# Kernel optimization log

Hardware: AMD Instinct MI355X
Metric: run time of the kernel (lower is better)

## Reference

```python
import jax, jax.numpy as jnp
import numpy as np

EPS = 1e-6
NUM_HEADS = 16


def _layer_norm(x):
    # LayerNorm32: fp32 layernorm, eps=1e-6, no affine params
    m = jnp.mean(x, axis=-1, keepdims=True)
    v = jnp.var(x, axis=-1, keepdims=True)
    return (x - m) * jax.lax.rsqrt(v + EPS)


def setup_inputs() -> dict:
    key = jax.random.key(0)
    ks = jax.random.split(key, 6)
    B, L, C = 4, 2048, 1024
    H = 4 * C
    s = 0.02
    return {
        "x": jax.random.normal(ks[0], (B, L, C), dtype=jnp.float32),
        "qkv_w": jax.random.normal(ks[1], (C, 3 * C), dtype=jnp.float32) * s,
        "qkv_b": jnp.zeros((3 * C,), dtype=jnp.float32),
        "proj_w": jax.random.normal(ks[2], (C, C), dtype=jnp.float32) * s,
        "proj_b": jnp.zeros((C,), dtype=jnp.float32),
        "fc1_w": jax.random.normal(ks[3], (C, H), dtype=jnp.float32) * s,
        "fc1_b": jnp.zeros((H,), dtype=jnp.float32),
        "fc2_w": jax.random.normal(ks[4], (H, C), dtype=jnp.float32) * s,
        "fc2_b": jnp.zeros((C,), dtype=jnp.float32),
    }


def _block(x, qkv_w, qkv_b, proj_w, proj_b, fc1_w, fc1_b, fc2_w, fc2_b):
    B, L, C = x.shape
    Hn = NUM_HEADS
    D = C // Hn

    # --- attention branch (pre-norm) ---
    h = _layer_norm(x)
    qkv = h @ qkv_w + qkv_b                      # [B, L, 3C]
    qkv = qkv.reshape(B, L, 3, Hn, D)
    q, k, v = qkv[:, :, 0], qkv[:, :, 1], qkv[:, :, 2]  # [B, L, Hn, D]
    scale = 1.0 / jnp.sqrt(jnp.asarray(D, dtype=x.dtype))
    logits = jnp.einsum("bqhd,bkhd->bhqk", q, k) * scale
    attn = jax.nn.softmax(logits, axis=-1)
    o = jnp.einsum("bhqk,bkhd->bqhd", attn, v).reshape(B, L, C)
    o = o @ proj_w + proj_b
    x = x + o

    # --- MLP branch (pre-norm) ---
    h = _layer_norm(x)
    h = jax.nn.gelu(h @ fc1_w + fc1_b, approximate=True)  # tanh GELU
    h = h @ fc2_w + fc2_b
    return x + h


def reference(x, qkv_w, qkv_b, proj_w, proj_b, fc1_w, fc1_b, fc2_w, fc2_b):
    return _block(x, qkv_w, qkv_b, proj_w, proj_b, fc1_w, fc1_b, fc2_w, fc2_b)
```

## Files before the change

### kernel.cpp

```cpp
#include <hip/hip_runtime.h>
#include <hip/hip_bf16.h>

typedef float f32x4 __attribute__((ext_vector_type(4)));
typedef __bf16 bf16x8 __attribute__((ext_vector_type(8)));
typedef unsigned short us8 __attribute__((ext_vector_type(8)));

#define MBYTE (1ull << 20)

#define QSCALE_LOG2E 0.18033688011112042f

__device__ __forceinline__ unsigned short f2bf(float f) {
    unsigned int u = __float_as_uint(f);
    u += 0x7fffu + ((u >> 16) & 1u);
    return (unsigned short)(u >> 16);
}

__device__ __forceinline__ float fast_exp2(float x) {
    return __builtin_amdgcn_exp2f(x);
}

__device__ __forceinline__ f32x4 mfma16(bf16x8 a, bf16x8 b, f32x4 c) {
    return __builtin_amdgcn_mfma_f32_16x16x32_bf16(a, b, c, 0, 0, 0);
}

__device__ __forceinline__ void gload16(const void* g, void* l) {
    __builtin_amdgcn_global_load_lds(
        (const __attribute__((address_space(1))) unsigned int*)g,
        (__attribute__((address_space(3))) unsigned int*)l, 16, 0, 0);
}

__global__ __launch_bounds__(256) void ln_kernel(const float* __restrict__ x,
                                                 unsigned short* __restrict__ out) {
    int row = blockIdx.x;
    int t = threadIdx.x;
    const float* xr = x + (size_t)row * 1024;
    float4 v = *(const float4*)(xr + t * 4);
    float s = v.x + v.y + v.z + v.w;
    float ss = v.x * v.x + v.y * v.y + v.z * v.z + v.w * v.w;
    #pragma unroll
    for (int off = 1; off < 64; off <<= 1) {
        s += __shfl_xor(s, off);
        ss += __shfl_xor(ss, off);
    }
    __shared__ float ps[4], pss[4];
    int wid = t >> 6, lane = t & 63;
    if (lane == 0) { ps[wid] = s; pss[wid] = ss; }
    __syncthreads();
    s = ps[0] + ps[1] + ps[2] + ps[3];
    ss = pss[0] + pss[1] + pss[2] + pss[3];
    float mean = s * (1.0f / 1024.0f);
    float var = ss * (1.0f / 1024.0f) - mean * mean;
    float rs = rsqrtf(var + 1e-6f);
    ushort4 ov;
    ov.x = f2bf((v.x - mean) * rs);
    ov.y = f2bf((v.y - mean) * rs);
    ov.z = f2bf((v.z - mean) * rs);
    ov.w = f2bf((v.w - mean) * rs);
    *(ushort4*)(out + (size_t)row * 1024 + t * 4) = ov;
}

__global__ __launch_bounds__(256) void convT_kernel(const float* __restrict__ W,
                                                    unsigned short* __restrict__ Wt,
                                                    int K, int N) {
    __shared__ float tile[32][33];
    int t = threadIdx.x;
    int tx = t & 31, ty = t >> 5;
    int bx = blockIdx.x, by = blockIdx.y;
    #pragma unroll
    for (int r = 0; r < 4; r++) {
        int row = by * 32 + ty + r * 8;
        int col = bx * 32 + tx;
        tile[ty + r * 8][tx] = W[(size_t)row * N + col];
    }
    __syncthreads();
    #pragma unroll
    for (int r = 0; r < 4; r++) {
        int orow = bx * 32 + ty + r * 8;
        int ocol = by * 32 + tx;
        Wt[(size_t)orow * K + ocol] = f2bf(tile[tx][ty + r * 8]);
    }
}

__global__ __launch_bounds__(256) void vT_kernel(const unsigned short* __restrict__ qkv,
                                                 unsigned short* __restrict__ vT) {
    __shared__ unsigned short tile[32][34];
    int t = threadIdx.x;
    int tx = t & 31, ty = t >> 5;
    int lt = blockIdx.x, dt = blockIdx.y, bh = blockIdx.z;
    int b = bh >> 4, h = bh & 15;
    const unsigned short* src = qkv + (size_t)(b * 2048 + lt * 32) * 3072 + 2048 + h * 64 + dt * 32;
    #pragma unroll
    for (int r = 0; r < 4; r++)
        tile[ty + r * 8][tx] = src[(size_t)(ty + r * 8) * 3072 + tx];
    __syncthreads();
    int perm = (lt & 1) * 32 + ((tx >> 2) & 3) * 8 + ((tx >> 4) & 1) * 4 + (tx & 3);
    unsigned short* dst = vT + ((size_t)bh * 64 + dt * 32) * 2048 + (size_t)(lt >> 1) * 64;
    #pragma unroll
    for (int r = 0; r < 4; r++)
        dst[(size_t)(ty + r * 8) * 2048 + perm] = tile[tx][ty + r * 8];
}

template <int EPI>
__global__ __launch_bounds__(256) void gemm_bt(const unsigned short* __restrict__ A,
                                               const unsigned short* __restrict__ Bt,
                                               const float* __restrict__ bias,
                                               const float* __restrict__ res,
                                               float* __restrict__ outF,
                                               unsigned short* __restrict__ outB,
                                               int M, int N, int K) {
    __shared__ __align__(16) unsigned short As[128 * 32];
    __shared__ __align__(16) unsigned short Bs[128 * 32];
    int t = threadIdx.x;
    int lane = t & 63, wid = t >> 6;

    int gx = gridDim.x;
    int nwg = gx * gridDim.y;
    int orig = blockIdx.y * gx + blockIdx.x;
    int cpx = nwg >> 3;
    int swz = (orig & 7) * cpx + (orig >> 3);
    int bm = swz / gx, bn = swz % gx;

    int wm = wid >> 1, wn = wid & 1;
    f32x4 acc[4][4] = {};

    int sub = lane >> 2;
    int chunk = lane & 3;
    const unsigned short* gA0 = A + (size_t)(bm * 128 + wid * 32 + sub) * K + chunk * 8;
    const unsigned short* gA1 = gA0 + (size_t)16 * K;
    const unsigned short* gB0 = Bt + (size_t)(bn * 128 + wid * 32 + sub) * K + chunk * 8;
    const unsigned short* gB1 = gB0 + (size_t)16 * K;
    unsigned short* lA0 = &As[(wid * 32) * 32];
    unsigned short* lA1 = &As[(wid * 32 + 16) * 32];
    unsigned short* lB0 = &Bs[(wid * 32) * 32];
    unsigned short* lB1 = &Bs[(wid * 32 + 16) * 32];

    for (int k0 = 0; k0 < K; k0 += 32) {
        __syncthreads();
        gload16(gA0 + k0, lA0);
        gload16(gA1 + k0, lA1);
        gload16(gB0 + k0, lB0);
        gload16(gB1 + k0, lB1);
        __syncthreads();
        bf16x8 af[4], bfr[4];
        #pragma unroll
        for (int m = 0; m < 4; m++)
            af[m] = *(const bf16x8*)&As[(wm * 64 + m * 16 + (lane & 15)) * 32 + (lane >> 4) * 8];
        #pragma unroll
        for (int n = 0; n < 4; n++)
            bfr[n] = *(const bf16x8*)&Bs[(wn * 64 + n * 16 + (lane & 15)) * 32 + (lane >> 4) * 8];
        #pragma unroll
        for (int m = 0; m < 4; m++)
            #pragma unroll
            for (int n = 0; n < 4; n++)
                acc[m][n] = mfma16(af[m], bfr[n], acc[m][n]);
    }

    #pragma unroll
    for (int m = 0; m < 4; m++) {
        #pragma unroll
        for (int n = 0; n < 4; n++) {
            int col = bn * 128 + wn * 64 + n * 16 + (lane & 15);
            float bv = bias[col];
            #pragma unroll
            for (int r = 0; r < 4; r++) {
                int row = bm * 128 + wm * 64 + m * 16 + (lane >> 4) * 4 + r;
                float val = acc[m][n][r] + bv;
                if (EPI == 0) {
                    if (col < 1024) val *= QSCALE_LOG2E;
                    outB[(size_t)row * N + col] = f2bf(val);
                } else if (EPI == 1) {
                    float g = 0.5f * val *
                              (1.0f + tanhf(0.7978845608028654f *
                                            (val + 0.044715f * val * val * val)));
                    outB[(size_t)row * N + col] = f2bf(g);
                } else {
                    outF[(size_t)row * N + col] = val + res[(size_t)row * N + col];
                }
            }
        }
    }
}

__global__ __launch_bounds__(256) void attn_kernel(const unsigned short* __restrict__ qkv,
                                                   const unsigned short* __restrict__ vT,
                                                   unsigned short* __restrict__ o) {
    int bid = blockIdx.x;
    int qb = bid & 31;
    int bh = bid >> 5;
    int b = bh >> 4, h = bh & 15;
    int t = threadIdx.x, lane = t & 63, wid = t >> 6;

    const unsigned short* base = qkv + (size_t)b * 2048 * 3072 + h * 64;
    const unsigned short* vbase = vT + (size_t)bh * 64 * 2048;

    __shared__ __align__(16) unsigned short Ks[64][72];
    __shared__ __align__(16) unsigned short Vs[64][72];

    int ql = lane & 15;
    int hi = lane >> 4;

    bf16x8 qf[2];
    {
        int qrow = qb * 64 + wid * 16 + ql;
        const unsigned short* qp = base + (size_t)qrow * 3072 + hi * 8;
        qf[0] = *(const bf16x8*)(qp);
        qf[1] = *(const bf16x8*)(qp + 32);
    }

    float m_r = -1e30f, lpart = 0.0f;
    f32x4 accO[4] = {};

    int srow = t >> 2;
    int scol = (t & 3) * 16;
    const unsigned short* kp = base + 1024 + (size_t)srow * 3072 + scol;
    const unsigned short* vp = vbase + (size_t)srow * 2048 + scol;

    us8 kr0 = *(const us8*)kp;
    us8 kr1 = *(const us8*)(kp + 8);
    us8 vr0 = *(const us8*)vp;
    us8 vr1 = *(const us8*)(vp + 8);

    for (int kt = 0; kt < 32; kt++) {
        __syncthreads();
        *(us8*)&Ks[srow][scol] = kr0;
        *(us8*)&Ks[srow][scol + 8] = kr1;
        *(us8*)&Vs[srow][scol] = vr0;
        *(us8*)&Vs[srow][scol + 8] = vr1;
        if (kt + 1 < 32) {
            const unsigned short* kpn = kp + (size_t)(kt + 1) * 64 * 3072;
            const unsigned short* vpn = vp + (kt + 1) * 64;
            kr0 = *(const us8*)kpn;
            kr1 = *(const us8*)(kpn + 8);
            vr0 = *(const us8*)vpn;
            vr1 = *(const us8*)(vpn + 8);
        }
        __syncthreads();

        f32x4 s0 = {}, s1 = {}, s2 = {}, s3 = {};
        #pragma unroll
        for (int c = 0; c < 2; c++) {
            bf16x8 a0 = *(const bf16x8*)&Ks[ 0 + ql][c * 32 + hi * 8];
            bf16x8 a1 = *(const bf16x8*)&Ks[16 + ql][c * 32 + hi * 8];
            bf16x8 a2 = *(const bf16x8*)&Ks[32 + ql][c * 32 + hi * 8];
            bf16x8 a3 = *(const bf16x8*)&Ks[48 + ql][c * 32 + hi * 8];
            s0 = mfma16(a0, qf[c], s0);
            s1 = mfma16(a1, qf[c], s1);
            s2 = mfma16(a2, qf[c], s2);
            s3 = mfma16(a3, qf[c], s3);
        }

        float mx = fmaxf(fmaxf(fmaxf(s0[0], s0[1]), fmaxf(s0[2], s0[3])),
                         fmaxf(fmaxf(s1[0], s1[1]), fmaxf(s1[2], s1[3])));
        mx = fmaxf(mx, fmaxf(fmaxf(s2[0], s2[1]), fmaxf(s2[2], s2[3])));
        mx = fmaxf(mx, fmaxf(fmaxf(s3[0], s3[1]), fmaxf(s3[2], s3[3])));
        if (!__all(mx <= m_r + 8.0f)) {
            float mm = fmaxf(mx, __shfl_xor(mx, 16));
            mm = fmaxf(mm, __shfl_xor(mm, 32));
            float mnew = fmaxf(m_r, mm);
            float corr = fast_exp2(m_r - mnew);
            m_r = mnew;
            lpart *= corr;
            #pragma unroll
            for (int r = 0; r < 4; r++) {
                float cq = __shfl(corr, hi * 4 + r);
                accO[0][r] *= cq; accO[1][r] *= cq;
                accO[2][r] *= cq; accO[3][r] *= cq;
            }
        }

        us8 pu0, pu1;
        #pragma unroll
        for (int j = 0; j < 4; j++) {
            float pa = fast_exp2(s0[j] - m_r);
            float pb = fast_exp2(s1[j] - m_r);
            float pc = fast_exp2(s2[j] - m_r);
            float pd = fast_exp2(s3[j] - m_r);
            lpart += (pa + pb) + (pc + pd);
            pu0[j] = f2bf(pa); pu0[4 + j] = f2bf(pb);
            pu1[j] = f2bf(pc); pu1[4 + j] = f2bf(pd);
        }
        bf16x8 paf0 = __builtin_bit_cast(bf16x8, pu0);
        bf16x8 paf1 = __builtin_bit_cast(bf16x8, pu1);

        #pragma unroll
        for (int nn = 0; nn < 4; nn++) {
            bf16x8 bv0 = *(const bf16x8*)&Vs[nn * 16 + ql][hi * 8];
            bf16x8 bv1 = *(const bf16x8*)&Vs[nn * 16 + ql][32 + hi * 8];
            accO[nn] = mfma16(paf0, bv0, accO[nn]);
            accO[nn] = mfma16(paf1, bv1, accO[nn]);
        }
    }

    lpart += __shfl_xor(lpart, 16);
    lpart += __shfl_xor(lpart, 32);
    float rinv = 1.0f / lpart;
    #pragma unroll
    for (int r = 0; r < 4; r++) {
        float rq = __shfl(rinv, hi * 4 + r);
        int row = qb * 64 + wid * 16 + hi * 4 + r;
        #pragma unroll
        for (int nn = 0; nn < 4; nn++) {
            int col = h * 64 + nn * 16 + ql;
            o[(size_t)(b * 2048 + row) * 1024 + col] = f2bf(accO[nn][r] * rq);
        }
    }
}

extern "C" void kernel_launch(void* const* d_in, const int* in_sizes, int n_in,
                              void* d_out, int out_size, void* d_ws, size_t ws_size,
                              hipStream_t stream) {
    const float* x      = (const float*)d_in[0];
    const float* qkv_w  = (const float*)d_in[1];
    const float* qkv_b  = (const float*)d_in[2];
    const float* proj_w = (const float*)d_in[3];
    const float* proj_b = (const float*)d_in[4];
    const float* fc1_w  = (const float*)d_in[5];
    const float* fc1_b  = (const float*)d_in[6];
    const float* fc2_w  = (const float*)d_in[7];
    const float* fc2_b  = (const float*)d_in[8];
    float* out = (float*)d_out;

    char* ws = (char*)d_ws;
    unsigned short* h_buf   = (unsigned short*)(ws + 0 * MBYTE);
    unsigned short* qkv_buf = (unsigned short*)(ws + 16 * MBYTE);
    unsigned short* o_buf   = (unsigned short*)(ws + 64 * MBYTE);
    float*          x2_buf  = (float*)(ws + 80 * MBYTE);
    unsigned short* vT_buf  = (unsigned short*)(ws + 80 * MBYTE);
    unsigned short* wqT     = (unsigned short*)(ws + 112 * MBYTE);
    unsigned short* wpT     = (unsigned short*)(ws + 118 * MBYTE);
    unsigned short* w1T     = (unsigned short*)(ws + 120 * MBYTE);
    unsigned short* w2T     = (unsigned short*)(ws + 128 * MBYTE);
    unsigned short* g_buf   = (unsigned short*)(ws + 16 * MBYTE);

    const int M = 8192;

    convT_kernel<<<dim3(3072 / 32, 1024 / 32), 256, 0, stream>>>(qkv_w, wqT, 1024, 3072);
    convT_kernel<<<dim3(1024 / 32, 1024 / 32), 256, 0, stream>>>(proj_w, wpT, 1024, 1024);
    convT_kernel<<<dim3(4096 / 32, 1024 / 32), 256, 0, stream>>>(fc1_w, w1T, 1024, 4096);
    convT_kernel<<<dim3(1024 / 32, 4096 / 32), 256, 0, stream>>>(fc2_w, w2T, 4096, 1024);

    ln_kernel<<<M, 256, 0, stream>>>(x, h_buf);

    gemm_bt<0><<<dim3(3072 / 128, M / 128), 256, 0, stream>>>(
        h_buf, wqT, qkv_b, nullptr, nullptr, qkv_buf, M, 3072, 1024);

    vT_kernel<<<dim3(64, 2, 64), 256, 0, stream>>>(qkv_buf, vT_buf);

    attn_kernel<<<dim3(32 * 64), 256, 0, stream>>>(qkv_buf, vT_buf, o_buf);

    gemm_bt<2><<<dim3(1024 / 128, M / 128), 256, 0, stream>>>(
        o_buf, wpT, proj_b, x, x2_buf, nullptr, M, 1024, 1024);

    ln_kernel<<<M, 256, 0, stream>>>(x2_buf, h_buf);

    gemm_bt<1><<<dim3(4096 / 128, M / 128), 256, 0, stream>>>(
        h_buf, w1T, fc1_b, nullptr, nullptr, g_buf, M, 4096, 1024);

    gemm_bt<2><<<dim3(1024 / 128, M / 128), 256, 0, stream>>>(
        g_buf, w2T, fc2_b, x2_buf, out, nullptr, M, 1024, 4096);
}
```

Baseline: 481.7 us.

## Load K/V tiles directly into LDS with global_load_lds and split layout

```diff
diff --git a/kernel.cpp b/kernel.cpp
--- a/kernel.cpp
+++ b/kernel.cpp
@@ -10,9 +10,8 @@
 #define QSCALE_LOG2E 0.18033688011112042f
 
 __device__ __forceinline__ unsigned short f2bf(float f) {
-    unsigned int u = __float_as_uint(f);
-    u += 0x7fffu + ((u >> 16) & 1u);
-    return (unsigned short)(u >> 16);
+    __bf16 h = (__bf16)f;
+    return __builtin_bit_cast(unsigned short, h);
 }
 
 __device__ __forceinline__ float fast_exp2(float x) {
@@ -193,8 +192,8 @@
     const unsigned short* base = qkv + (size_t)b * 2048 * 3072 + h * 64;
     const unsigned short* vbase = vT + (size_t)bh * 64 * 2048;
 
-    __shared__ __align__(16) unsigned short Ks[64][72];
-    __shared__ __align__(16) unsigned short Vs[64][72];
+    __shared__ __align__(16) unsigned short Ks[2][64][32];
+    __shared__ __align__(16) unsigned short Vs[2][64][32];
 
     int ql = lane & 15;
     int hi = lane >> 4;
@@ -210,39 +209,32 @@
     float m_r = -1e30f, lpart = 0.0f;
     f32x4 accO[4] = {};
 
-    int srow = t >> 2;
-    int scol = (t & 3) * 16;
-    const unsigned short* kp = base + 1024 + (size_t)srow * 3072 + scol;
-    const unsigned short* vp = vbase + (size_t)srow * 2048 + scol;
-
-    us8 kr0 = *(const us8*)kp;
-    us8 kr1 = *(const us8*)(kp + 8);
-    us8 vr0 = *(const us8*)vp;
-    us8 vr1 = *(const us8*)(vp + 8);
+    int srow = wid * 16 + (lane >> 2);
+    int schunk = (lane & 3) * 8;
+    const unsigned short* gk = base + 1024 + (size_t)srow * 3072 + schunk;
+    const unsigned short* gv = vbase + (size_t)srow * 2048 + schunk;
+    unsigned short* lK0 = &Ks[0][wid * 16][0];
+    unsigned short* lK1 = &Ks[1][wid * 16][0];
+    unsigned short* lV0 = &Vs[0][wid * 16][0];
+    unsigned short* lV1 = &Vs[1][wid * 16][0];
 
     for (int kt = 0; kt < 32; kt++) {
         __syncthreads();
-        *(us8*)&Ks[srow][scol] = kr0;
-        *(us8*)&Ks[srow][scol + 8] = kr1;
-        *(us8*)&Vs[srow][scol] = vr0;
-        *(us8*)&Vs[srow][scol + 8] = vr1;
-        if (kt + 1 < 32) {
-            const unsigned short* kpn = kp + (size_t)(kt + 1) * 64 * 3072;
-            const unsigned short* vpn = vp + (kt + 1) * 64;
-            kr0 = *(const us8*)kpn;
-            kr1 = *(const us8*)(kpn + 8);
-            vr0 = *(const us8*)vpn;
-            vr1 = *(const us8*)(vpn + 8);
-        }
+        gload16(gk, lK0);
+        gload16(gk + 32, lK1);
+        gload16(gv, lV0);
+        gload16(gv + 32, lV1);
+        gk += (size_t)64 * 3072;
+        gv += 64;
         __syncthreads();
 
         f32x4 s0 = {}, s1 = {}, s2 = {}, s3 = {};
         #pragma unroll
         for (int c = 0; c < 2; c++) {
-            bf16x8 a0 = *(const bf16x8*)&Ks[ 0 + ql][c * 32 + hi * 8];
-            bf16x8 a1 = *(const bf16x8*)&Ks[16 + ql][c * 32 + hi * 8];
-            bf16x8 a2 = *(const bf16x8*)&Ks[32 + ql][c * 32 + hi * 8];
-            bf16x8 a3 = *(const bf16x8*)&Ks[48 + ql][c * 32 + hi * 8];
+            bf16x8 a0 = *(const bf16x8*)&Ks[c][ 0 + ql][hi * 8];
+            bf16x8 a1 = *(const bf16x8*)&Ks[c][16 + ql][hi * 8];
+            bf16x8 a2 = *(const bf16x8*)&Ks[c][32 + ql][hi * 8];
+            bf16x8 a3 = *(const bf16x8*)&Ks[c][48 + ql][hi * 8];
             s0 = mfma16(a0, qf[c], s0);
             s1 = mfma16(a1, qf[c], s1);
             s2 = mfma16(a2, qf[c], s2);
@@ -284,8 +276,8 @@
 
         #pragma unroll
         for (int nn = 0; nn < 4; nn++) {
-            bf16x8 bv0 = *(const bf16x8*)&Vs[nn * 16 + ql][hi * 8];
-            bf16x8 bv1 = *(const bf16x8*)&Vs[nn * 16 + ql][32 + hi * 8];
+            bf16x8 bv0 = *(const bf16x8*)&Vs[0][nn * 16 + ql][hi * 8];
+            bf16x8 bv1 = *(const bf16x8*)&Vs[1][nn * 16 + ql][hi * 8];
             accO[nn] = mfma16(paf0, bv0, accO[nn]);
             accO[nn] = mfma16(paf1, bv1, accO[nn]);
         }
```

Result: no change. 472.4 us (-1.9%).
